# Kernel optimization log

Hardware: AMD Instinct MI355X
Metric: run time of the kernel (lower is better)

The kernel has to match this reference:

```python
import jax, jax.numpy as jnp
import numpy as np

KSZ = 1  # kernel_size from init_kwargs


def setup_inputs() -> dict:
    key = jax.random.key(0)
    k1, k2 = jax.random.split(key)
    S, B, H, W = 10, 8, 512, 512
    predicted = jax.random.normal(k1, (S, B, H, W), dtype=jnp.float32)
    target = jax.random.uniform(k2, (B, S, H, W), dtype=jnp.float32)
    mask = jnp.ones((B, S, H, W), dtype=jnp.float32)
    return {"predicted": predicted, "target": target, "mask": mask}


def reference(predicted, target, mask):
    # predicted: [S,B,H,W] -> [B,S,H,W] (torch .permute(1,0,2,3))
    pred = jnp.transpose(predicted, (1, 0, 2, 3))
    # use_weights=False -> weights = ones_like(target); mask unused
    weights = jnp.ones_like(target)
    H, W = target.shape[-2], target.shape[-1]

    # The torch loop does a running strict-< min over shifts (x,y) in row-major
    # order, seeded with the unshifted (0,0) loss. Final selection therefore is
    # the FIRST shift (in order [(0,0)] + loop order) achieving the global min,
    # which is exactly jnp.argmin's first-occurrence tie-breaking.
    shifts = [(0, 0)] + [(x, y) for x in range(-KSZ, KSZ + 1)
                         for y in range(-KSZ, KSZ + 1)]

    pad = jnp.pad(pred, ((0, 0), (0, 0), (KSZ, KSZ), (KSZ, KSZ)))
    valid = jnp.pad(jnp.ones((H, W), dtype=bool),
                    ((KSZ, KSZ), (KSZ, KSZ)))  # in-bounds map

    cands, losses = [], []
    for (x, y) in shifts:
        # candidate at pixel (i,j) is predicted[i+x, j+y]
        c = pad[..., KSZ + x:KSZ + x + H, KSZ + y:KSZ + y + W]
        v = valid[KSZ + x:KSZ + x + H, KSZ + y:KSZ + y + W]
        l = jnp.abs((target - c) * weights)
        losses.append(jnp.where(v, l, jnp.inf))
        cands.append(c)

    cands = jnp.stack(cands)    # [n_shifts, B, S, H, W]
    losses = jnp.stack(losses)  # [n_shifts, B, S, H, W]

    idx = jnp.argmin(losses, axis=0)                       # [B,S,H,W]
    kpred = jnp.take_along_axis(cands, idx[None], axis=0)[0]
    return jnp.transpose(kpred, (1, 0, 2, 3))  # back to [S,B,H,W]
```

## Files before the change

### kernel.cpp

```cpp
#include <hip/hip_runtime.h>

#define SS 10
#define BB 8
#define HH 512
#define WW 512

__global__ __launch_bounds__(256) void shiftpred_kernel(
    const float* __restrict__ pred,
    const float* __restrict__ targ,
    float* __restrict__ out)
{
    const int W4 = WW / 4;
    int tid = blockIdx.x * blockDim.x + threadIdx.x;

    int wq = tid & (W4 - 1);
    int h  = (tid >> 7) & (HH - 1);
    int sb = tid >> 16;
    if (sb >= SS * BB) return;

    int s = sb >> 3;
    int b = sb & 7;
    int wb = wq << 2;

    const float* pplane = pred + (size_t)sb * (HH * WW);
    const float* tplane = targ + (size_t)(b * SS + s) * (HH * WW);

    float4 t4 = *reinterpret_cast<const float4*>(tplane + h * WW + wb);
    float tv[4] = {t4.x, t4.y, t4.z, t4.w};

    float v[3][6];
    bool rowvalid[3];
    #pragma unroll
    for (int xi = 0; xi < 3; ++xi) {
        int hh = h + xi - 1;
        bool rv = (hh >= 0) && (hh < HH);
        rowvalid[xi] = rv;
        int hc = rv ? hh : h;
        const float* rp = pplane + hc * WW + wb;
        float4 c4 = *reinterpret_cast<const float4*>(rp);
        float lft = (wb > 0)        ? rp[-1] : rp[0];
        float rgt = (wb + 4 < WW)   ? rp[4]  : rp[3];
        v[xi][0] = lft;  v[xi][1] = c4.x; v[xi][2] = c4.y;
        v[xi][3] = c4.z; v[xi][4] = c4.w; v[xi][5] = rgt;
    }

    float res[4];
    #pragma unroll
    for (int j = 0; j < 4; ++j) {
        int w = wb + j;
        float bestc = v[1][j + 1];
        float bestl = fabsf(tv[j] - bestc);
        #pragma unroll
        for (int xi = 0; xi < 3; ++xi) {
            #pragma unroll
            for (int yi = 0; yi < 3; ++yi) {
                float c = v[xi][j + yi];
                float l = fabsf(tv[j] - c);
                bool valid = rowvalid[xi] && ((unsigned)(w + yi - 1) < (unsigned)WW);
                if (valid && l < bestl) { bestl = l; bestc = c; }
            }
        }
        res[j] = bestc;
    }

    float4 o4 = make_float4(res[0], res[1], res[2], res[3]);
    *reinterpret_cast<float4*>(out + (size_t)sb * (HH * WW) + h * WW + wb) = o4;
}

extern "C" void kernel_launch(void* const* d_in, const int* in_sizes, int n_in,
                              void* d_out, int out_size, void* d_ws, size_t ws_size,
                              hipStream_t stream) {
    const float* pred = (const float*)d_in[0];
    const float* targ = (const float*)d_in[1];
    float* out = (float*)d_out;

    const int total_threads = SS * BB * HH * (WW / 4);
    const int block = 256;
    const int grid = (total_threads + block - 1) / block;
    shiftpred_kernel<<<grid, block, 0, stream>>>(pred, targ, out);
}
```

Baseline: 242.5 us.

## Compute 4x4 output tile per thread and use sentinel padding instead of validity checks

Each thread now handles four rows of four pixels, loading six predicted rows once and reusing them across the 3x3 neighbourhoods of all four output rows. This cuts redundant row loads from three per output row to 1.5. Out-of-bounds neighbours are replaced with a large sentinel value so the per-candidate validity test is dropped from the inner loop. The costs are more registers per thread and a quarter as many threads. The sentinel could also change tie behaviour if real data ever reached such large magnitudes.

```diff
diff --git a/kernel.cpp b/kernel.cpp
--- a/kernel.cpp
+++ b/kernel.cpp
@@ -4,6 +4,20 @@
 #define BB 8
 #define HH 512
 #define WW 512
+#define BIGV 3.0e38f
+
+__device__ __forceinline__ void load_row(float dst[6], const float* __restrict__ rp,
+                                         int wb, bool rv) {
+    float4 c4 = *reinterpret_cast<const float4*>(rp);
+    float lft = (wb > 0)      ? rp[-1] : BIGV;
+    float rgt = (wb + 4 < WW) ? rp[4]  : BIGV;
+    dst[0] = rv ? lft  : BIGV;
+    dst[1] = rv ? c4.x : BIGV;
+    dst[2] = rv ? c4.y : BIGV;
+    dst[3] = rv ? c4.z : BIGV;
+    dst[4] = rv ? c4.w : BIGV;
+    dst[5] = rv ? rgt  : BIGV;
+}
 
 __global__ __launch_bounds__(256) void shiftpred_kernel(
     const float* __restrict__ pred,
@@ -11,60 +25,60 @@
     float* __restrict__ out)
 {
     const int W4 = WW / 4;
+    const int H4 = HH / 4;
     int tid = blockIdx.x * blockDim.x + threadIdx.x;
 
     int wq = tid & (W4 - 1);
-    int h  = (tid >> 7) & (HH - 1);
-    int sb = tid >> 16;
+    int hq = (tid >> 7) & (H4 - 1);
+    int sb = tid >> 14;
     if (sb >= SS * BB) return;
 
     int s = sb >> 3;
     int b = sb & 7;
     int wb = wq << 2;
+    int h0 = hq << 2;
 
     const float* pplane = pred + (size_t)sb * (HH * WW);
     const float* tplane = targ + (size_t)(b * SS + s) * (HH * WW);
+    float*       oplane = out  + (size_t)sb * (HH * WW);
 
-    float4 t4 = *reinterpret_cast<const float4*>(tplane + h * WW + wb);
-    float tv[4] = {t4.x, t4.y, t4.z, t4.w};
-
-    float v[3][6];
-    bool rowvalid[3];
-    #pragma unroll
-    for (int xi = 0; xi < 3; ++xi) {
-        int hh = h + xi - 1;
-        bool rv = (hh >= 0) && (hh < HH);
-        rowvalid[xi] = rv;
-        int hc = rv ? hh : h;
-        const float* rp = pplane + hc * WW + wb;
-        float4 c4 = *reinterpret_cast<const float4*>(rp);
-        float lft = (wb > 0)        ? rp[-1] : rp[0];
-        float rgt = (wb + 4 < WW)   ? rp[4]  : rp[3];
-        v[xi][0] = lft;  v[xi][1] = c4.x; v[xi][2] = c4.y;
-        v[xi][3] = c4.z; v[xi][4] = c4.w; v[xi][5] = rgt;
+    float v[6][6];
+    {
+        bool rv0 = (h0 - 1) >= 0;
+        bool rv5 = (h0 + 4) < HH;
+        int  hc0 = rv0 ? (h0 - 1) : 0;
+        int  hc5 = rv5 ? (h0 + 4) : 0;
+        load_row(v[0], pplane + hc0 * WW + wb, wb, rv0);
+        #pragma unroll
+        for (int r = 1; r <= 4; ++r)
+            load_row(v[r], pplane + (h0 + r - 1) * WW + wb, wb, true);
+        load_row(v[5], pplane + hc5 * WW + wb, wb, rv5);
     }
 
-    float res[4];
     #pragma unroll
-    for (int j = 0; j < 4; ++j) {
-        int w = wb + j;
-        float bestc = v[1][j + 1];
-        float bestl = fabsf(tv[j] - bestc);
+    for (int r = 0; r < 4; ++r) {
+        float4 t4 = *reinterpret_cast<const float4*>(tplane + (h0 + r) * WW + wb);
+        float tv[4] = {t4.x, t4.y, t4.z, t4.w};
+        float res[4];
         #pragma unroll
-        for (int xi = 0; xi < 3; ++xi) {
+        for (int j = 0; j < 4; ++j) {
+            float t = tv[j];
+            float bestc = v[r + 1][j + 1];
+            float bestl = fabsf(t - bestc);
             #pragma unroll
-            for (int yi = 0; yi < 3; ++yi) {
-                float c = v[xi][j + yi];
-                float l = fabsf(tv[j] - c);
-                bool valid = rowvalid[xi] && ((unsigned)(w + yi - 1) < (unsigned)WW);
-                if (valid && l < bestl) { bestl = l; bestc = c; }
+            for (int xi = 0; xi < 3; ++xi) {
+                #pragma unroll
+                for (int yi = 0; yi < 3; ++yi) {
+                    float c = v[r + xi][j + yi];
+                    float l = fabsf(t - c);
+                    if (l < bestl) { bestl = l; bestc = c; }
+                }
             }
+            res[j] = bestc;
         }
-        res[j] = bestc;
+        float4 o4 = make_float4(res[0], res[1], res[2], res[3]);
+        *reinterpret_cast<float4*>(oplane + (h0 + r) * WW + wb) = o4;
     }
-
-    float4 o4 = make_float4(res[0], res[1], res[2], res[3]);
-    *reinterpret_cast<float4*>(out + (size_t)sb * (HH * WW) + h * WW + wb) = o4;
 }
 
 extern "C" void kernel_launch(void* const* d_in, const int* in_sizes, int n_in,
@@ -74,7 +88,7 @@
     const float* targ = (const float*)d_in[1];
     float* out = (float*)d_out;
 
-    const int total_threads = SS * BB * HH * (WW / 4);
+    const int total_threads = SS * BB * (HH / 4) * (WW / 4);
     const int block = 256;
     const int grid = (total_threads + block - 1) / block;
     shiftpred_kernel<<<grid, block, 0, stream>>>(pred, targ, out);
```

Measured after the change: 253.2 us. +4.4%, slower.

## Persistent wave-per-row kernel with software prefetch and shuffle halos

Applied to the files above, without the earlier changes.

Each wavefront now handles one full image row, eight floats per lane, across five planes in a fixed 2048-block grid. Block indices are swizzled across groups of eight, and the next plane's loads are issued before the current plane is computed. Horizontal halo values come from lane shuffles instead of extra scalar loads. Out-of-range neighbours are replaced by a huge sentinel value rather than per-candidate validity checks. This is meant to cut redundant memory transactions and hide load latency, at the cost of higher register pressure from double-buffered tiles.

```diff
diff --git a/kernel.cpp b/kernel.cpp
--- a/kernel.cpp
+++ b/kernel.cpp
@@ -4,67 +4,107 @@
 #define BB 8
 #define HH 512
 #define WW 512
+#define PLANE (HH * WW)
+#define BIGV 3.0e38f
 
-__global__ __launch_bounds__(256) void shiftpred_kernel(
+#define NBLK 2048
+#define NITER 5
+
+__global__ __launch_bounds__(256, 4) void shiftpred_kernel(
     const float* __restrict__ pred,
     const float* __restrict__ targ,
     float* __restrict__ out)
 {
-    const int W4 = WW / 4;
-    int tid = blockIdx.x * blockDim.x + threadIdx.x;
+    int bid = blockIdx.x;
+    int swz = (bid & 7) * (NBLK / 8) + (bid >> 3);
 
-    int wq = tid & (W4 - 1);
-    int h  = (tid >> 7) & (HH - 1);
-    int sb = tid >> 16;
-    if (sb >= SS * BB) return;
+    int wv   = swz * 4 + (int)(threadIdx.x >> 6);
+    int lane = (int)(threadIdx.x & 63);
+    int h    = wv & (HH - 1);
+    int sb0  = wv >> 9;
+    int w0   = lane << 3;
 
-    int s = sb >> 3;
-    int b = sb & 7;
-    int wb = wq << 2;
+    const bool hm_ok = (h > 0);
+    const bool hp_ok = (h < HH - 1);
+    const size_t roff  = (size_t)h * WW + w0;
+    const size_t roffm = roff - WW;
+    const size_t roffp = roff + WW;
 
-    const float* pplane = pred + (size_t)sb * (HH * WW);
-    const float* tplane = targ + (size_t)(b * SS + s) * (HH * WW);
+    const float4 big4 = make_float4(BIGV, BIGV, BIGV, BIGV);
 
-    float4 t4 = *reinterpret_cast<const float4*>(tplane + h * WW + wb);
-    float tv[4] = {t4.x, t4.y, t4.z, t4.w};
+    auto tile_load = [&](int sb, float4& m0, float4& m1, float4& c0, float4& c1,
+                         float4& p0, float4& p1, float4& t0, float4& t1) {
+        int s = sb >> 3, b = sb & 7;
+        const float* pp = pred + (size_t)sb * PLANE;
+        const float* tp = targ + (size_t)(b * SS + s) * PLANE;
+        c0 = *reinterpret_cast<const float4*>(pp + roff);
+        c1 = *reinterpret_cast<const float4*>(pp + roff + 4);
+        if (hm_ok) {
+            m0 = *reinterpret_cast<const float4*>(pp + roffm);
+            m1 = *reinterpret_cast<const float4*>(pp + roffm + 4);
+        } else { m0 = big4; m1 = big4; }
+        if (hp_ok) {
+            p0 = *reinterpret_cast<const float4*>(pp + roffp);
+            p1 = *reinterpret_cast<const float4*>(pp + roffp + 4);
+        } else { p0 = big4; p1 = big4; }
+        t0 = *reinterpret_cast<const float4*>(tp + roff);
+        t1 = *reinterpret_cast<const float4*>(tp + roff + 4);
+    };
 
-    float v[3][6];
-    bool rowvalid[3];
+    auto tile_compute = [&](int sb, float4 m0, float4 m1, float4 c0, float4 c1,
+                            float4 p0, float4 p1, float4 t0, float4 t1) {
+        float v[3][10];
+        v[0][1] = m0.x; v[0][2] = m0.y; v[0][3] = m0.z; v[0][4] = m0.w;
+        v[0][5] = m1.x; v[0][6] = m1.y; v[0][7] = m1.z; v[0][8] = m1.w;
+        v[1][1] = c0.x; v[1][2] = c0.y; v[1][3] = c0.z; v[1][4] = c0.w;
+        v[1][5] = c1.x; v[1][6] = c1.y; v[1][7] = c1.z; v[1][8] = c1.w;
+        v[2][1] = p0.x; v[2][2] = p0.y; v[2][3] = p0.z; v[2][4] = p0.w;
+        v[2][5] = p1.x; v[2][6] = p1.y; v[2][7] = p1.z; v[2][8] = p1.w;
+        float lm = __shfl_up(m1.w, 1);  float rm = __shfl_down(m0.x, 1);
+        float lc = __shfl_up(c1.w, 1);  float rc = __shfl_down(c0.x, 1);
+        float lp = __shfl_up(p1.w, 1);  float rp = __shfl_down(p0.x, 1);
+        bool e0 = (lane == 0), e63 = (lane == 63);
+        v[0][0] = e0 ? BIGV : lm;  v[0][9] = e63 ? BIGV : rm;
+        v[1][0] = e0 ? BIGV : lc;  v[1][9] = e63 ? BIGV : rc;
+        v[2][0] = e0 ? BIGV : lp;  v[2][9] = e63 ? BIGV : rp;
+
+        float tv[8]  = {t0.x, t0.y, t0.z, t0.w, t1.x, t1.y, t1.z, t1.w};
+        float res[8];
+        #pragma unroll
+        for (int j = 0; j < 8; ++j) {
+            float t = tv[j];
+            float bestc = v[1][j + 1];
+            float bestl = fabsf(t - bestc);
+            #pragma unroll
+            for (int xi = 0; xi < 3; ++xi) {
+                #pragma unroll
+                for (int yi = 0; yi < 3; ++yi) {
+                    float c = v[xi][j + yi];
+                    float l = fabsf(t - c);
+                    if (l < bestl) { bestl = l; bestc = c; }
+                }
+            }
+            res[j] = bestc;
+        }
+        float* op = out + (size_t)sb * PLANE + roff;
+        *reinterpret_cast<float4*>(op)     = make_float4(res[0], res[1], res[2], res[3]);
+        *reinterpret_cast<float4*>(op + 4) = make_float4(res[4], res[5], res[6], res[7]);
+    };
+
+    float4 cm0, cm1, cc0, cc1, cp0, cp1, ct0, ct1;
+    float4 nm0, nm1, nc0, nc1, np0, np1, nt0, nt1;
+
+    tile_load(sb0, cm0, cm1, cc0, cc1, cp0, cp1, ct0, ct1);
     #pragma unroll
-    for (int xi = 0; xi < 3; ++xi) {
-        int hh = h + xi - 1;
-        bool rv = (hh >= 0) && (hh < HH);
-        rowvalid[xi] = rv;
-        int hc = rv ? hh : h;
-        const float* rp = pplane + hc * WW + wb;
-        float4 c4 = *reinterpret_cast<const float4*>(rp);
-        float lft = (wb > 0)        ? rp[-1] : rp[0];
-        float rgt = (wb + 4 < WW)   ? rp[4]  : rp[3];
-        v[xi][0] = lft;  v[xi][1] = c4.x; v[xi][2] = c4.y;
-        v[xi][3] = c4.z; v[xi][4] = c4.w; v[xi][5] = rgt;
+    for (int it = 0; it < NITER; ++it) {
+        int sb = sb0 + (it << 4);
+        if (it < NITER - 1)
+            tile_load(sb0 + ((it + 1) << 4),
+                      nm0, nm1, nc0, nc1, np0, np1, nt0, nt1);
+        tile_compute(sb, cm0, cm1, cc0, cc1, cp0, cp1, ct0, ct1);
+        cm0 = nm0; cm1 = nm1; cc0 = nc0; cc1 = nc1;
+        cp0 = np0; cp1 = np1; ct0 = nt0; ct1 = nt1;
     }
-
-    float res[4];
-    #pragma unroll
-    for (int j = 0; j < 4; ++j) {
-        int w = wb + j;
-        float bestc = v[1][j + 1];
-        float bestl = fabsf(tv[j] - bestc);
-        #pragma unroll
-        for (int xi = 0; xi < 3; ++xi) {
-            #pragma unroll
-            for (int yi = 0; yi < 3; ++yi) {
-                float c = v[xi][j + yi];
-                float l = fabsf(tv[j] - c);
-                bool valid = rowvalid[xi] && ((unsigned)(w + yi - 1) < (unsigned)WW);
-                if (valid && l < bestl) { bestl = l; bestc = c; }
-            }
-        }
-        res[j] = bestc;
-    }
-
-    float4 o4 = make_float4(res[0], res[1], res[2], res[3]);
-    *reinterpret_cast<float4*>(out + (size_t)sb * (HH * WW) + h * WW + wb) = o4;
 }
 
 extern "C" void kernel_launch(void* const* d_in, const int* in_sizes, int n_in,
@@ -73,9 +113,5 @@
     const float* pred = (const float*)d_in[0];
     const float* targ = (const float*)d_in[1];
     float* out = (float*)d_out;
-
-    const int total_threads = SS * BB * HH * (WW / 4);
-    const int block = 256;
-    const int grid = (total_threads + block - 1) / block;
-    shiftpred_kernel<<<grid, block, 0, stream>>>(pred, targ, out);
+    shiftpred_kernel<<<NBLK, 256, 0, stream>>>(pred, targ, out);
 }
```

Result: slower. 247.5 us (+2.1%).
